# Kernel optimization log

Measured on AMD Instinct MI355X. Metric: run time of the kernel, lower is better.

Reference implementation:

```python
import jax, jax.numpy as jnp
import numpy as np

D_MODEL = 1024
NUM_HEADS = 16
HEAD_DIM = D_MODEL // NUM_HEADS
THETA = 10000.0
B, S = 1, 2048


def setup_inputs() -> dict:
    key = jax.random.key(0)
    ks = jax.random.split(key, 7)
    sc = 0.02
    return {
        "query": jax.random.normal(ks[0], (B, S, D_MODEL), jnp.float32),
        "key": jax.random.normal(ks[1], (B, S, D_MODEL), jnp.float32),
        "value": jax.random.normal(ks[2], (B, S, D_MODEL), jnp.float32),
        "qkv_w": jax.random.normal(ks[3], (3 * D_MODEL, D_MODEL), jnp.float32) * sc,
        "qkv_b": jax.random.normal(ks[4], (3 * D_MODEL,), jnp.float32) * sc,
        "out_w": jax.random.normal(ks[5], (D_MODEL, D_MODEL), jnp.float32) * sc,
        "out_b": jax.random.normal(ks[6], (D_MODEL,), jnp.float32) * sc,
    }


def _rope_cos_sin(seq_len, head_dim, dtype):
    # freqs_for='lang': inv_freq = theta^(-2i/d), i = 0..d/2-1
    inv_freq = 1.0 / (THETA ** (jnp.arange(0, head_dim, 2, dtype=jnp.float32) / head_dim))
    t = jnp.arange(seq_len, dtype=jnp.float32)
    freqs = jnp.outer(t, inv_freq)                      # [S, d/2]
    emb = jnp.concatenate([freqs, freqs], axis=-1)      # [S, d] (non-interleaved)
    return jnp.cos(emb).astype(dtype), jnp.sin(emb).astype(dtype)


def _rotate_half(x):
    half = x.shape[-1] // 2
    return jnp.concatenate([-x[..., half:], x[..., :half]], axis=-1)


def reference(query, key, value, qkv_w, qkv_b, out_w, out_b):
    # NOTE: module computes q,k,v all from `query` (key/value args unused).
    b, s, d = query.shape
    qkv = query @ qkv_w.T + qkv_b                       # [B,S,3D]
    qkv = qkv.reshape(b, s, 3, NUM_HEADS, HEAD_DIM)
    qkv = jnp.transpose(qkv, (2, 0, 3, 1, 4))           # [3,B,H,S,hd]
    q, k, v = qkv[0], qkv[1], qkv[2]

    cos, sin = _rope_cos_sin(s, HEAD_DIM, query.dtype)  # [S,hd]
    q = q * cos + _rotate_half(q) * sin
    k = k * cos + _rotate_half(k) * sin

    scale = 1.0 / np.sqrt(HEAD_DIM)
    scores = jnp.einsum('bhqd,bhkd->bhqk', q, k) * scale
    attn = jax.nn.softmax(scores, axis=-1)
    ctx = jnp.einsum('bhqk,bhkd->bhqd', attn, v)        # [B,H,S,hd]
    ctx = jnp.transpose(ctx, (0, 2, 1, 3)).reshape(b, s, d)
    return ctx @ out_w.T + out_b
```

## Files before the change

kernel.cpp:

```cpp
#include <hip/hip_runtime.h>
#include <math.h>
#include <stdint.h>

#define SEQ 2048
#define DM  1024
#define NH  16
#define HD  64
#define TRI 3072
#define NSPLIT 2

typedef _Float16 half8 __attribute__((ext_vector_type(8)));
typedef _Float16 half4 __attribute__((ext_vector_type(4)));
typedef __fp16 fp16x2 __attribute__((ext_vector_type(2)));
typedef float f32x4 __attribute__((ext_vector_type(4)));

#define GLOAD_LDS16(g, l)                                       \
  __builtin_amdgcn_global_load_lds(                             \
      (__attribute__((address_space(1))) void*)(g),             \
      (__attribute__((address_space(3))) void*)(l), 16, 0, 0)

#define QSCALE 0.18033688011112042f

__global__ __launch_bounds__(256)
void cvt3(const float* __restrict__ s1, const float* __restrict__ s2,
          const float* __restrict__ s3, _Float16* __restrict__ d1,
          _Float16* __restrict__ d2, _Float16* __restrict__ d3,
          float2* __restrict__ tab, int n1, int n2) {
  int b = blockIdx.x;
  if (b >= 6144) {
    int i = (b - 6144) * 256 + threadIdx.x;
    int s = i >> 5, d = i & 31;
    float inv = exp2f((float)d * -0.4152410118609203f);
    float ang = (float)s * inv;
    float sn, cs;
    sincosf(ang, &sn, &cs);
    tab[i] = make_float2(cs, sn);
    return;
  }
  int i = (b * 256 + threadIdx.x) * 4;
  const float* s; _Float16* d;
  if (i < n1)            { s = s1; d = d1; }
  else if (i < n1 + n2)  { s = s2; d = d2; i -= n1; }
  else                   { s = s3; d = d3; i -= n1 + n2; }
  float4 v = *(const float4*)(s + i);
  union { _Float16 h[4]; uint2 u; } pk;
  pk.h[0] = (_Float16)v.x; pk.h[1] = (_Float16)v.y;
  pk.h[2] = (_Float16)v.z; pk.h[3] = (_Float16)v.w;
  *(uint2*)(d + i) = pk.u;
}

__global__ __launch_bounds__(256)
void gemm_qkv(const _Float16* __restrict__ A, const _Float16* __restrict__ B,
              const float* __restrict__ bias, const float2* __restrict__ tab,
              _Float16* __restrict__ Qo, _Float16* __restrict__ Ko,
              _Float16* __restrict__ Vo) {
  constexpr int K = DM;
  __shared__ _Float16 As[2][64 * 32];
  __shared__ _Float16 Bs[2][128 * 32];

  const int t = threadIdx.x, lane = t & 63, wv = t >> 6;
  const int l15 = lane & 15, l4 = lane >> 4;
  const int wr = wv >> 1, wc = wv & 1;
  const int bm = blockIdx.y * 64, bn = blockIdx.x * 128;

  auto stage = [&](int buf, int k0) {
    {
      int c = t;
      GLOAD_LDS16(A + (size_t)(bm + (c >> 2)) * K + k0 + (c & 3) * 8,
                  (char*)&As[buf][wv * 512]);
    }
    #pragma unroll
    for (int i = 0; i < 2; ++i) {
      int c = t + i * 256;
      GLOAD_LDS16(B + (size_t)(bn + (c >> 2)) * K + k0 + (c & 3) * 8,
                  (char*)&Bs[buf][(i * 256 + wv * 64) * 8]);
    }
  };

  f32x4 acc[2][4] = {};
  stage(0, 0);
  __syncthreads();

  const int nk = K / 32;
  for (int s = 0; s < nk; ++s) {
    int cur = s & 1;
    if (s + 1 < nk) stage(cur ^ 1, (s + 1) * 32);
    half8 af[2], bf[4];
    #pragma unroll
    for (int mf = 0; mf < 2; ++mf)
      af[mf] = *(const half8*)&As[cur][(wr * 32 + mf * 16 + l15) * 32 + l4 * 8];
    #pragma unroll
    for (int nf = 0; nf < 4; ++nf)
      bf[nf] = *(const half8*)&Bs[cur][(wc * 64 + nf * 16 + l15) * 32 + l4 * 8];
    __builtin_amdgcn_s_setprio(1);
    #pragma unroll
    for (int mf = 0; mf < 2; ++mf)
      #pragma unroll
      for (int nf = 0; nf < 4; ++nf)
        acc[mf][nf] = __builtin_amdgcn_mfma_f32_16x16x32_f16(
            af[mf], bf[nf], acc[mf][nf], 0, 0, 0);
    __builtin_amdgcn_s_setprio(0);
    __syncthreads();
  }

  const int sec = bn >> 10;
  float bv[4];
  #pragma unroll
  for (int nf = 0; nf < 4; ++nf) bv[nf] = bias[bn + wc * 64 + nf * 16 + l15];

  if (sec == 0) {
    #pragma unroll
    for (int mf = 0; mf < 2; ++mf)
      #pragma unroll
      for (int r = 0; r < 4; ++r) {
        int row = bm + wr * 32 + mf * 16 + l4 * 4 + r;
        float v0 = acc[mf][0][r] + bv[0];
        float v1 = acc[mf][1][r] + bv[1];
        float v2 = acc[mf][2][r] + bv[2];
        float v3 = acc[mf][3][r] + bv[3];
        float2 cs0 = tab[row * 32 + l15];
        float2 cs1 = tab[row * 32 + 16 + l15];
        float a0 = (v0 * cs0.x - v2 * cs0.y) * QSCALE;
        float a2 = (v2 * cs0.x + v0 * cs0.y) * QSCALE;
        float a1 = (v1 * cs1.x - v3 * cs1.y) * QSCALE;
        float a3 = (v3 * cs1.x + v1 * cs1.y) * QSCALE;
        _Float16* cr = Qo + (size_t)row * DM + bn + wc * 64 + l15;
        cr[0]  = (_Float16)a0; cr[16] = (_Float16)a1;
        cr[32] = (_Float16)a2; cr[48] = (_Float16)a3;
      }
  } else if (sec == 1) {
    const int hh = ((bn - 1024) >> 6) + wc;
    const int e = l15 & 7, hi = l15 >> 3;
    #pragma unroll
    for (int mf = 0; mf < 2; ++mf)
      #pragma unroll
      for (int r = 0; r < 4; ++r) {
        int row = bm + wr * 32 + mf * 16 + l4 * 4 + r;
        float v0 = acc[mf][0][r] + bv[0];
        float v1 = acc[mf][1][r] + bv[1];
        float v2 = acc[mf][2][r] + bv[2];
        float v3 = acc[mf][3][r] + bv[3];
        float2 cs0 = tab[row * 32 + l15];
        float2 cs1 = tab[row * 32 + 16 + l15];
        float a0 = v0 * cs0.x - v2 * cs0.y;
        float a2 = v2 * cs0.x + v0 * cs0.y;
        float a1 = v1 * cs1.x - v3 * cs1.y;
        float a3 = v3 * cs1.x + v1 * cs1.y;
        int kk = row & 63, kseg = row >> 6, ks7 = kk & 7;
        size_t base = ((size_t)(hh * 32 + kseg) * 64 + kk) * 64;
        Ko[base + (((0 + hi) ^ ks7) * 8) + e] = (_Float16)a0;
        Ko[base + (((2 + hi) ^ ks7) * 8) + e] = (_Float16)a1;
        Ko[base + (((4 + hi) ^ ks7) * 8) + e] = (_Float16)a2;
        Ko[base + (((6 + hi) ^ ks7) * 8) + e] = (_Float16)a3;
      }
  } else {
    const int hh = ((bn - 2048) >> 6) + wc;
    #pragma unroll
    for (int mf = 0; mf < 2; ++mf) {
      int row0 = bm + wr * 32 + mf * 16 + l4 * 4;
      int kk0 = row0 & 63, kseg = row0 >> 6;
      #pragma unroll
      for (int nf = 0; nf < 4; ++nf) {
        int d = nf * 16 + l15;
        union { _Float16 hh4[4]; uint2 u; } pk;
        #pragma unroll
        for (int r = 0; r < 4; ++r)
          pk.hh4[r] = (_Float16)(acc[mf][nf][r] + bv[nf]);
        size_t off = ((size_t)(hh * 32 + kseg) * 64 + d) * 64 +
                     (((kk0 >> 3) ^ (d & 7)) * 8) + (kk0 & 7);
        *(uint2*)(Vo + off) = pk.u;
      }
    }
  }
}

__global__ __launch_bounds__(256)
void gemm_out(const _Float16* __restrict__ A, const _Float16* __restrict__ B,
              const float* __restrict__ bias, float* __restrict__ C) {
  constexpr int K = DM, N = DM;
  __shared__ _Float16 As[2][64 * 32];
  __shared__ _Float16 Bs[2][128 * 32];

  const int t = threadIdx.x, lane = t & 63, wv = t >> 6;
  const int l15 = lane & 15, l4 = lane >> 4;
  const int wr = wv >> 1, wc = wv & 1;
  const int bm = blockIdx.y * 64, bn = blockIdx.x * 128;

  auto stage = [&](int buf, int k0) {
    {
      int c = t;
      GLOAD_LDS16(A + (size_t)(bm + (c >> 2)) * K + k0 + (c & 3) * 8,
                  (char*)&As[buf][wv * 512]);
    }
    #pragma unroll
    for (int i = 0; i < 2; ++i) {
      int c = t + i * 256;
      GLOAD_LDS16(B + (size_t)(bn + (c >> 2)) * K + k0 + (c & 3) * 8,
                  (char*)&Bs[buf][(i * 256 + wv * 64) * 8]);
    }
  };

  f32x4 acc[2][4] = {};
  stage(0, 0);
  __syncthreads();

  const int nk = K / 32;
  for (int s = 0; s < nk; ++s) {
    int cur = s & 1;
    if (s + 1 < nk) stage(cur ^ 1, (s + 1) * 32);
    half8 af[2], bf[4];
    #pragma unroll
    for (int mf = 0; mf < 2; ++mf)
      af[mf] = *(const half8*)&As[cur][(wr * 32 + mf * 16 + l15) * 32 + l4 * 8];
    #pragma unroll
    for (int nf = 0; nf < 4; ++nf)
      bf[nf] = *(const half8*)&Bs[cur][(wc * 64 + nf * 16 + l15) * 32 + l4 * 8];
    __builtin_amdgcn_s_setprio(1);
    #pragma unroll
    for (int mf = 0; mf < 2; ++mf)
      #pragma unroll
      for (int nf = 0; nf < 4; ++nf)
        acc[mf][nf] = __builtin_amdgcn_mfma_f32_16x16x32_f16(
            af[mf], bf[nf], acc[mf][nf], 0, 0, 0);
    __builtin_amdgcn_s_setprio(0);
    __syncthreads();
  }

  float bv[4];
  #pragma unroll
  for (int nf = 0; nf < 4; ++nf) bv[nf] = bias[bn + wc * 64 + nf * 16 + l15];
  #pragma unroll
  for (int mf = 0; mf < 2; ++mf)
    #pragma unroll
    for (int r = 0; r < 4; ++r) {
      int row = bm + wr * 32 + mf * 16 + l4 * 4 + r;
      float* cr = C + (size_t)row * N + bn + wc * 64 + l15;
      cr[0]  = acc[mf][0][r] + bv[0];
      cr[16] = acc[mf][1][r] + bv[1];
      cr[32] = acc[mf][2][r] + bv[2];
      cr[48] = acc[mf][3][r] + bv[3];
    }
}

__global__ __launch_bounds__(256)
void attn_f16(const _Float16* __restrict__ Qg, const _Float16* __restrict__ Kg,
              const _Float16* __restrict__ Vg, _Float16* __restrict__ po,
              float* __restrict__ pl) {
  __shared__ _Float16 Kl[2][64 * 64];
  __shared__ _Float16 Vt[2][64 * 64];

  const int t = threadIdx.x, lane = t & 63, wv = t >> 6;
  const int l15 = lane & 15, l4 = lane >> 4;
  const int bid = blockIdx.x;
  const int c = bid & 31, qb = bid >> 5;
  const int h = c & 15, z = c >> 4;
  const int q0 = qb * 64;
  const int seg0 = z * (SEQ / NSPLIT / 64);

  const _Float16* Qp = Qg + h * HD;
  const _Float16* Kbase = Kg + (size_t)h * 32 * 4096;
  const _Float16* Vbase = Vg + (size_t)h * 32 * 4096;

  half8 qf[2];
  {
    const _Float16* qrow = Qp + (size_t)(q0 + wv * 16 + l15) * DM;
    qf[0] = *(const half8*)(qrow + l4 * 8);
    qf[1] = *(const half8*)(qrow + 32 + l4 * 8);
  }

  auto issueKV = [&](int buf, int seg) {
    const _Float16* ks = Kbase + (size_t)seg * 4096;
    const _Float16* vs = Vbase + (size_t)seg * 4096;
    GLOAD_LDS16(ks + (size_t)t * 8,         (char*)&Kl[buf][(wv * 64) * 8]);
    GLOAD_LDS16(ks + (size_t)(t + 256) * 8, (char*)&Kl[buf][(256 + wv * 64) * 8]);
    GLOAD_LDS16(vs + (size_t)t * 8,         (char*)&Vt[buf][(wv * 64) * 8]);
    GLOAD_LDS16(vs + (size_t)(t + 256) * 8, (char*)&Vt[buf][(256 + wv * 64) * 8]);
  };

  f32x4 lacc = {0.f, 0.f, 0.f, 0.f};
  f32x4 o[4] = {};

  issueKV(0, seg0);

  const int NT = SEQ / NSPLIT / 64;
  #pragma unroll 2
  for (int tt = 0; tt < NT; ++tt) {
    const int cur = tt & 1;
    asm volatile("s_waitcnt vmcnt(0)" ::: "memory");
    __builtin_amdgcn_s_barrier();
    __builtin_amdgcn_sched_barrier(0);
    if (tt + 1 < NT) issueKV(cur ^ 1, seg0 + tt + 1);

    f32x4 sT[4] = {};
    __builtin_amdgcn_s_setprio(1);
    #pragma unroll
    for (int ds = 0; ds < 2; ++ds)
      #pragma unroll
      for (int mf = 0; mf < 4; ++mf) {
        int r = mf * 16 + l15;
        int cb = ds * 4 + l4;
        half8 kf = *(const half8*)(&Kl[cur][r * 64 + ((cb ^ (r & 7)) * 8)]);
        sT[mf] = __builtin_amdgcn_mfma_f32_16x16x32_f16(kf, qf[ds], sT[mf], 0, 0, 0);
      }
    __builtin_amdgcn_s_setprio(0);

    half4 pA[4];
    #pragma unroll
    for (int mf = 0; mf < 4; ++mf) {
      f32x4 p;
      #pragma unroll
      for (int r = 0; r < 4; ++r) p[r] = exp2f(sT[mf][r]);
      lacc += p;
      union { fp16x2 h2[2]; half4 a; } pu;
      pu.h2[0] = __builtin_amdgcn_cvt_pkrtz(p[0], p[1]);
      pu.h2[1] = __builtin_amdgcn_cvt_pkrtz(p[2], p[3]);
      pA[mf] = pu.a;
    }

    __builtin_amdgcn_s_setprio(1);
    #pragma unroll
    for (int mf = 0; mf < 4; ++mf) {
      int cc = ((mf * 2 + (l4 >> 1)) ^ (l15 & 7)) * 16 + (l4 & 1) * 8;
      #pragma unroll
      for (int nf = 0; nf < 4; ++nf) {
        half4 vb = *(const half4*)((char*)Vt[cur] + (nf * 16 + l15) * 128 + cc);
        o[nf] = __builtin_amdgcn_mfma_f32_16x16x16f16(pA[mf], vb, o[nf], 0, 0, 0);
      }
    }
    __builtin_amdgcn_s_setprio(0);
  }

  float lv = (lacc[0] + lacc[1]) + (lacc[2] + lacc[3]);
  lv += __shfl_xor(lv, 16);
  lv += __shfl_xor(lv, 32);
  _Float16* pz = po + (size_t)z * SEQ * DM;
  #pragma unroll
  for (int nf = 0; nf < 4; ++nf)
    #pragma unroll
    for (int r = 0; r < 4; ++r) {
      int row = q0 + wv * 16 + l4 * 4 + r;
      int col = h * HD + nf * 16 + l15;
      pz[(size_t)row * DM + col] = (_Float16)o[nf][r];
    }
  if (l4 == 0) {
    int q = q0 + wv * 16 + l15;
    pl[(z * NH + h) * SEQ + q] = lv;
  }
}

__global__ __launch_bounds__(256)
void merge2(const _Float16* __restrict__ po, const float* __restrict__ pl,
            _Float16* __restrict__ ctx) {
  int e = (blockIdx.x * 256 + threadIdx.x) * 8;
  int s = e >> 10, h = (e & 1023) >> 6;
  int idx = h * SEQ + s;
  float inv = 1.0f / (pl[idx] + pl[NH * SEQ + idx]);
  half8 a = *(const half8*)(po + e);
  half8 b = *(const half8*)(po + (size_t)SEQ * DM + e);
  half8 o;
  #pragma unroll
  for (int j = 0; j < 8; ++j)
    o[j] = (_Float16)(((float)a[j] + (float)b[j]) * inv);
  *(half8*)(ctx + e) = o;
}

extern "C" void kernel_launch(void* const* d_in, const int* in_sizes, int n_in,
                              void* d_out, int out_size, void* d_ws, size_t ws_size,
                              hipStream_t stream) {
  const float* query = (const float*)d_in[0];
  const float* qkv_w = (const float*)d_in[3];
  const float* qkv_b = (const float*)d_in[4];
  const float* out_w = (const float*)d_in[5];
  const float* out_b = (const float*)d_in[6];
  float* out = (float*)d_out;

  _Float16* Aq   = (_Float16*)d_ws;
  _Float16* Wqkv = Aq + (size_t)SEQ * DM;
  _Float16* Wout = Wqkv + (size_t)TRI * DM;
  _Float16* Qb   = Wout + (size_t)DM * DM;
  _Float16* Kb   = Qb + (size_t)SEQ * DM;
  _Float16* Vb   = Kb + (size_t)SEQ * DM;
  _Float16* ctx  = Vb + (size_t)SEQ * DM;
  float2*   tab  = (float2*)(ctx + (size_t)SEQ * DM);
  _Float16* po = (_Float16*)d_ws;
  float*    pl = (float*)((char*)d_ws + (8u << 20));

  cvt3<<<6400, 256, 0, stream>>>(query, qkv_w, out_w, Aq, Wqkv, Wout, tab,
                                 SEQ * DM, TRI * DM);

  gemm_qkv<<<dim3(TRI / 128, SEQ / 64), 256, 0, stream>>>(
      Aq, Wqkv, qkv_b, tab, Qb, Kb, Vb);

  attn_f16<<<(SEQ / 64) * NH * NSPLIT, 256, 0, stream>>>(Qb, Kb, Vb, po, pl);

  merge2<<<SEQ * DM / 8 / 256, 256, 0, stream>>>(po, pl, ctx);

  gemm_out<<<dim3(DM / 128, SEQ / 64), 256, 0, stream>>>(ctx, Wout, out_b, out);
}
```

Measured before the change: 97.73 us.

## Split attention keys four ways and give each block 128 query rows

```diff
diff --git a/kernel.cpp b/kernel.cpp
--- a/kernel.cpp
+++ b/kernel.cpp
@@ -7,7 +7,7 @@
 #define NH  16
 #define HD  64
 #define TRI 3072
-#define NSPLIT 2
+#define NSPLIT 4
 
 typedef _Float16 half8 __attribute__((ext_vector_type(8)));
 typedef _Float16 half4 __attribute__((ext_vector_type(4)));
@@ -244,28 +244,29 @@
 
 __global__ __launch_bounds__(256)
 void attn_f16(const _Float16* __restrict__ Qg, const _Float16* __restrict__ Kg,
-              const _Float16* __restrict__ Vg, _Float16* __restrict__ po,
-              float* __restrict__ pl) {
+              const _Float16* __restrict__ Vg, _Float16* __restrict__ poA,
+              _Float16* __restrict__ po3, float* __restrict__ pl) {
   __shared__ _Float16 Kl[2][64 * 64];
   __shared__ _Float16 Vt[2][64 * 64];
 
   const int t = threadIdx.x, lane = t & 63, wv = t >> 6;
   const int l15 = lane & 15, l4 = lane >> 4;
   const int bid = blockIdx.x;
-  const int c = bid & 31, qb = bid >> 5;
+  const int c = bid & 63, qb = bid >> 6;
   const int h = c & 15, z = c >> 4;
-  const int q0 = qb * 64;
+  const int q0 = qb * 128;
   const int seg0 = z * (SEQ / NSPLIT / 64);
 
   const _Float16* Qp = Qg + h * HD;
   const _Float16* Kbase = Kg + (size_t)h * 32 * 4096;
   const _Float16* Vbase = Vg + (size_t)h * 32 * 4096;
 
-  half8 qf[2];
-  {
-    const _Float16* qrow = Qp + (size_t)(q0 + wv * 16 + l15) * DM;
-    qf[0] = *(const half8*)(qrow + l4 * 8);
-    qf[1] = *(const half8*)(qrow + 32 + l4 * 8);
+  half8 qf[2][2];
+  #pragma unroll
+  for (int qk = 0; qk < 2; ++qk) {
+    const _Float16* qrow = Qp + (size_t)(q0 + wv * 32 + qk * 16 + l15) * DM;
+    qf[qk][0] = *(const half8*)(qrow + l4 * 8);
+    qf[qk][1] = *(const half8*)(qrow + 32 + l4 * 8);
   }
 
   auto issueKV = [&](int buf, int seg) {
@@ -277,8 +278,8 @@
     GLOAD_LDS16(vs + (size_t)(t + 256) * 8, (char*)&Vt[buf][(256 + wv * 64) * 8]);
   };
 
-  f32x4 lacc = {0.f, 0.f, 0.f, 0.f};
-  f32x4 o[4] = {};
+  f32x4 lacc[2] = {};
+  f32x4 o[2][4] = {};
 
   issueKV(0, seg0);
 
@@ -291,7 +292,7 @@
     __builtin_amdgcn_sched_barrier(0);
     if (tt + 1 < NT) issueKV(cur ^ 1, seg0 + tt + 1);
 
-    f32x4 sT[4] = {};
+    f32x4 sT[2][4] = {};
     __builtin_amdgcn_s_setprio(1);
     #pragma unroll
     for (int ds = 0; ds < 2; ++ds)
@@ -300,22 +301,25 @@
         int r = mf * 16 + l15;
         int cb = ds * 4 + l4;
         half8 kf = *(const half8*)(&Kl[cur][r * 64 + ((cb ^ (r & 7)) * 8)]);
-        sT[mf] = __builtin_amdgcn_mfma_f32_16x16x32_f16(kf, qf[ds], sT[mf], 0, 0, 0);
+        sT[0][mf] = __builtin_amdgcn_mfma_f32_16x16x32_f16(kf, qf[0][ds], sT[0][mf], 0, 0, 0);
+        sT[1][mf] = __builtin_amdgcn_mfma_f32_16x16x32_f16(kf, qf[1][ds], sT[1][mf], 0, 0, 0);
       }
     __builtin_amdgcn_s_setprio(0);
 
-    half4 pA[4];
-    #pragma unroll
-    for (int mf = 0; mf < 4; ++mf) {
-      f32x4 p;
-      #pragma unroll
-      for (int r = 0; r < 4; ++r) p[r] = exp2f(sT[mf][r]);
-      lacc += p;
-      union { fp16x2 h2[2]; half4 a; } pu;
-      pu.h2[0] = __builtin_amdgcn_cvt_pkrtz(p[0], p[1]);
-      pu.h2[1] = __builtin_amdgcn_cvt_pkrtz(p[2], p[3]);
-      pA[mf] = pu.a;
-    }
+    half4 pA[2][4];
+    #pragma unroll
+    for (int qk = 0; qk < 2; ++qk)
+      #pragma unroll
+      for (int mf = 0; mf < 4; ++mf) {
+        f32x4 p;
+        #pragma unroll
+        for (int r = 0; r < 4; ++r) p[r] = exp2f(sT[qk][mf][r]);
+        lacc[qk] += p;
+        union { fp16x2 h2[2]; half4 a; } pu;
+        pu.h2[0] = __builtin_amdgcn_cvt_pkrtz(p[0], p[1]);
+        pu.h2[1] = __builtin_amdgcn_cvt_pkrtz(p[2], p[3]);
+        pA[qk][mf] = pu.a;
+      }
 
     __builtin_amdgcn_s_setprio(1);
     #pragma unroll
@@ -324,43 +328,52 @@
       #pragma unroll
       for (int nf = 0; nf < 4; ++nf) {
         half4 vb = *(const half4*)((char*)Vt[cur] + (nf * 16 + l15) * 128 + cc);
-        o[nf] = __builtin_amdgcn_mfma_f32_16x16x16f16(pA[mf], vb, o[nf], 0, 0, 0);
+        o[0][nf] = __builtin_amdgcn_mfma_f32_16x16x16f16(pA[0][mf], vb, o[0][nf], 0, 0, 0);
+        o[1][nf] = __builtin_amdgcn_mfma_f32_16x16x16f16(pA[1][mf], vb, o[1][nf], 0, 0, 0);
       }
     }
     __builtin_amdgcn_s_setprio(0);
   }
 
-  float lv = (lacc[0] + lacc[1]) + (lacc[2] + lacc[3]);
-  lv += __shfl_xor(lv, 16);
-  lv += __shfl_xor(lv, 32);
-  _Float16* pz = po + (size_t)z * SEQ * DM;
-  #pragma unroll
-  for (int nf = 0; nf < 4; ++nf)
-    #pragma unroll
-    for (int r = 0; r < 4; ++r) {
-      int row = q0 + wv * 16 + l4 * 4 + r;
-      int col = h * HD + nf * 16 + l15;
-      pz[(size_t)row * DM + col] = (_Float16)o[nf][r];
-    }
-  if (l4 == 0) {
-    int q = q0 + wv * 16 + l15;
-    pl[(z * NH + h) * SEQ + q] = lv;
+  _Float16* pz = (z < 3) ? (poA + (size_t)z * SEQ * DM) : po3;
+  #pragma unroll
+  for (int qk = 0; qk < 2; ++qk) {
+    float lv = (lacc[qk][0] + lacc[qk][1]) + (lacc[qk][2] + lacc[qk][3]);
+    lv += __shfl_xor(lv, 16);
+    lv += __shfl_xor(lv, 32);
+    #pragma unroll
+    for (int nf = 0; nf < 4; ++nf)
+      #pragma unroll
+      for (int r = 0; r < 4; ++r) {
+        int row = q0 + wv * 32 + qk * 16 + l4 * 4 + r;
+        int col = h * HD + nf * 16 + l15;
+        pz[(size_t)row * DM + col] = (_Float16)o[qk][nf][r];
+      }
+    if (l4 == 0) {
+      int q = q0 + wv * 32 + qk * 16 + l15;
+      pl[(z * NH + h) * SEQ + q] = lv;
+    }
   }
 }
 
 __global__ __launch_bounds__(256)
-void merge2(const _Float16* __restrict__ po, const float* __restrict__ pl,
-            _Float16* __restrict__ ctx) {
+void merge4(const _Float16* __restrict__ poA, const _Float16* __restrict__ po3,
+            const float* __restrict__ pl, _Float16* __restrict__ ctx) {
   int e = (blockIdx.x * 256 + threadIdx.x) * 8;
   int s = e >> 10, h = (e & 1023) >> 6;
   int idx = h * SEQ + s;
-  float inv = 1.0f / (pl[idx] + pl[NH * SEQ + idx]);
-  half8 a = *(const half8*)(po + e);
-  half8 b = *(const half8*)(po + (size_t)SEQ * DM + e);
+  float L = pl[idx] + pl[NH * SEQ + idx] + pl[2 * NH * SEQ + idx] +
+            pl[3 * NH * SEQ + idx];
+  float inv = 1.0f / L;
+  half8 a = *(const half8*)(poA + e);
+  half8 b = *(const half8*)(poA + (size_t)SEQ * DM + e);
+  half8 cc = *(const half8*)(poA + 2 * (size_t)SEQ * DM + e);
+  half8 d = *(const half8*)(po3 + e);
   half8 o;
   #pragma unroll
   for (int j = 0; j < 8; ++j)
-    o[j] = (_Float16)(((float)a[j] + (float)b[j]) * inv);
+    o[j] = (_Float16)((((float)a[j] + (float)b[j]) +
+                       ((float)cc[j] + (float)d[j])) * inv);
   *(half8*)(ctx + e) = o;
 }
 
@@ -374,16 +387,18 @@
   const float* out_b = (const float*)d_in[6];
   float* out = (float*)d_out;
 
-  _Float16* Aq   = (_Float16*)d_ws;
-  _Float16* Wqkv = Aq + (size_t)SEQ * DM;
-  _Float16* Wout = Wqkv + (size_t)TRI * DM;
-  _Float16* Qb   = Wout + (size_t)DM * DM;
-  _Float16* Kb   = Qb + (size_t)SEQ * DM;
-  _Float16* Vb   = Kb + (size_t)SEQ * DM;
-  _Float16* ctx  = Vb + (size_t)SEQ * DM;
-  float2*   tab  = (float2*)(ctx + (size_t)SEQ * DM);
-  _Float16* po = (_Float16*)d_ws;
-  float*    pl = (float*)((char*)d_ws + (8u << 20));
+  char* ws = (char*)d_ws;
+  _Float16* Aq   = (_Float16*)ws;
+  _Float16* Wqkv = (_Float16*)(ws + (4u << 20));
+  _Float16* Qb   = (_Float16*)(ws + (12u << 20));
+  _Float16* Kb   = (_Float16*)(ws + (16u << 20));
+  _Float16* Vb   = (_Float16*)(ws + (20u << 20));
+  _Float16* ctx  = (_Float16*)(ws + (24u << 20));
+  float2*   tab  = (float2*)(ws + (28u << 20));
+  _Float16* Wout = (_Float16*)(ws + (28u << 20) + (512u << 10));
+  float*    pl   = (float*)(ws + (30u << 20) + (512u << 10));
+  _Float16* poA  = (_Float16*)ws;
+  _Float16* po3  = ctx;
 
   cvt3<<<6400, 256, 0, stream>>>(query, qkv_w, out_w, Aq, Wqkv, Wout, tab,
                                  SEQ * DM, TRI * DM);
@@ -391,9 +406,10 @@
   gemm_qkv<<<dim3(TRI / 128, SEQ / 64), 256, 0, stream>>>(
       Aq, Wqkv, qkv_b, tab, Qb, Kb, Vb);
 
-  attn_f16<<<(SEQ / 64) * NH * NSPLIT, 256, 0, stream>>>(Qb, Kb, Vb, po, pl);
-
-  merge2<<<SEQ * DM / 8 / 256, 256, 0, stream>>>(po, pl, ctx);
+  attn_f16<<<(SEQ / 128) * NH * NSPLIT, 256, 0, stream>>>(
+      Qb, Kb, Vb, poA, po3, pl);
+
+  merge4<<<SEQ * DM / 8 / 256, 256, 0, stream>>>(poA, po3, pl, ctx);
 
   gemm_out<<<dim3(DM / 128, SEQ / 64), 256, 0, stream>>>(ctx, Wout, out_b, out);
 }
```

Measured after the change: 99.34 us. No clear change (+1.7%).
